# Kernel tuning notes

Hardware: AMD Instinct MI355X
Metric: run time of the kernel (lower is better)

## Reference

```python
import jax, jax.numpy as jnp
import numpy as np

N_NODES = 10000
N_EDGES = 160000
IN_DIM = 512
HID = 256
HEADS = 4
OUT_DIM = 512
NEG_SLOPE = 0.2  # PyG GATConv default


def _glorot(key, shape):
    fan_in, fan_out = shape[0], shape[-1]
    lim = jnp.sqrt(6.0 / (fan_in + fan_out))
    return jax.random.uniform(key, shape, jnp.float32, -lim, lim)


def setup_inputs() -> dict:
    key = jax.random.key(0)
    ks = jax.random.split(key, 16)
    x = jax.random.normal(ks[0], (N_NODES, IN_DIM), jnp.float32)
    edge_index = jax.random.randint(ks[1], (2, N_EDGES), 0, N_NODES, jnp.int64)
    # layer 1: GATConv(512 -> 256, heads=4, concat) -> out 1024
    W1 = _glorot(ks[2], (IN_DIM, HEADS * HID))
    att_src1 = _glorot(ks[3], (HEADS, HID))
    att_dst1 = _glorot(ks[4], (HEADS, HID))
    b1 = jnp.zeros((HEADS * HID,), jnp.float32)
    # layer 2: GATConv(1024 -> 256, heads=4, concat) -> out 1024
    W2 = _glorot(ks[5], (HEADS * HID, HEADS * HID))
    att_src2 = _glorot(ks[6], (HEADS, HID))
    att_dst2 = _glorot(ks[7], (HEADS, HID))
    b2 = jnp.zeros((HEADS * HID,), jnp.float32)
    # final fc: 1024 -> 512
    fcW = _glorot(ks[8], (HEADS * HID, OUT_DIM))
    fcb = jnp.zeros((OUT_DIM,), jnp.float32)
    return dict(x=x, edge_index=edge_index, W1=W1, att_src1=att_src1,
                att_dst1=att_dst1, b1=b1, W2=W2, att_src2=att_src2,
                att_dst2=att_dst2, b2=b2, fcW=fcW, fcb=fcb)


def gat_conv(x, src, dst, W, att_src, att_dst, bias):
    # x: [N, F_in]; src/dst: [E] (self-loops already included)
    N = x.shape[0]
    h = (x @ W).reshape(N, HEADS, HID)                       # [N, H, C]
    a_src = jnp.sum(h * att_src, axis=-1)                    # [N, H]
    a_dst = jnp.sum(h * att_dst, axis=-1)                    # [N, H]
    e = jax.nn.leaky_relu(a_src[src] + a_dst[dst], NEG_SLOPE)  # [E, H]
    # numerically stable segment softmax over destination nodes
    m = jax.ops.segment_max(e, dst, num_segments=N)          # [N, H]
    e = jnp.exp(e - m[dst])
    s = jax.ops.segment_sum(e, dst, num_segments=N)          # [N, H]
    alpha = e / (s[dst] + 1e-16)                             # [E, H]
    msg = alpha[:, :, None] * h[src]                         # [E, H, C]
    out = jax.ops.segment_sum(msg, dst, num_segments=N)      # [N, H, C]
    return out.reshape(N, HEADS * HID) + bias


def reference(x, edge_index, W1, att_src1, att_dst1, b1,
              W2, att_src2, att_dst2, b2, fcW, fcb):
    N = x.shape[0]
    loops = jnp.arange(N, dtype=edge_index.dtype)
    src = jnp.concatenate([edge_index[0], loops])  # PyG add_self_loops=True
    dst = jnp.concatenate([edge_index[1], loops])
    h = gat_conv(x, src, dst, W1, att_src1, att_dst1, b1)
    h = jax.nn.relu(h)  # dropout is identity in eval mode
    h = gat_conv(h, src, dst, W2, att_src2, att_dst2, b2)
    h = jax.nn.relu(h)
    return h @ fcW + fcb
```

## Files before the change

### kernel.cpp

```cpp
#include <hip/hip_runtime.h>
#include <hip/hip_bf16.h>

#define NN 10000
#define NE 160000
#define NET 170000
#define IN_DIM 512
#define D1 1024
#define HEADS 4
#define HID 256
#define OUT_DIM 512
#define NEG_SLOPE 0.2f

typedef __attribute__((ext_vector_type(8))) short bf16x8;
typedef __attribute__((ext_vector_type(4))) float f32x4;

__device__ inline float b2f(unsigned short b) {
    union { unsigned u; float f; } x; x.u = ((unsigned)b) << 16; return x.f;
}
__device__ inline unsigned short f2b(float f) {
    union { float f; unsigned u; } x; x.f = f;
    unsigned u = x.u;
    unsigned r = u + 0x7FFFu + ((u >> 16) & 1u);
    return (unsigned short)(r >> 16);
}
__device__ inline float lrelu(float v) { return v > 0.f ? v : NEG_SLOPE * v; }

__global__ void init_kernel(const int* ei32, int* flag, int* counts, int* cursor) {
    int i = blockIdx.x * blockDim.x + threadIdx.x;
    if (i < NN) { counts[i] = 0; cursor[i] = 0; }
    if (blockIdx.x == 0) {
        __shared__ int nz;
        if (threadIdx.x == 0) nz = 0;
        __syncthreads();
        int acc = 0;
        for (int k = threadIdx.x; k < 500; k += 256) acc |= ei32[2 * k + 1];
        if (acc) atomicOr(&nz, 1);
        __syncthreads();
        if (threadIdx.x == 0) flag[0] = (nz == 0) ? 1 : 0;
    }
}

__device__ inline void load_edge(const void* ei, int f64, int e, int& s, int& d) {
    if (f64) {
        const long long* p = (const long long*)ei;
        s = (int)p[e]; d = (int)p[NE + e];
    } else {
        const int* p = (const int*)ei;
        s = p[e]; d = p[NE + e];
    }
}

__global__ void count_kernel(const void* ei, const int* flag, int* counts) {
    int e = blockIdx.x * blockDim.x + threadIdx.x;
    if (e >= NET) return;
    int s, d;
    if (e < NE) load_edge(ei, *flag, e, s, d);
    else d = e - NE;
    atomicAdd(&counts[d], 1);
}

__global__ __launch_bounds__(256) void scan_kernel(const int* counts, int* indptr) {
    __shared__ int part[256];
    int t = threadIdx.x;
    int base = t * 40;
    int local[40];
    int sum = 0;
#pragma unroll
    for (int k = 0; k < 40; k++) {
        int i = base + k;
        int c = (i < NN) ? counts[i] : 0;
        local[k] = sum;
        sum += c;
    }
    part[t] = sum;
    __syncthreads();
    for (int off = 1; off < 256; off <<= 1) {
        int v = (t >= off) ? part[t - off] : 0;
        __syncthreads();
        part[t] += v;
        __syncthreads();
    }
    int excl = part[t] - sum;
#pragma unroll
    for (int k = 0; k < 40; k++) {
        int i = base + k;
        if (i < NN) indptr[i] = excl + local[k];
    }
    if (t == 255) indptr[NN] = part[255];
}

__global__ void fill_kernel(const void* ei, const int* flag, const int* indptr,
                            int* cursor, int* csr_src) {
    int e = blockIdx.x * blockDim.x + threadIdx.x;
    if (e >= NET) return;
    int s, d;
    if (e < NE) load_edge(ei, *flag, e, s, d);
    else { s = e - NE; d = s; }
    int pos = indptr[d] + atomicAdd(&cursor[d], 1);
    csr_src[pos] = s;
}

__device__ void tpose_tile(const float* __restrict__ in, unsigned short* __restrict__ out,
                           int R, int C, int bx, int by) {
    __shared__ float tile[32][33];
    int tx = threadIdx.x & 31, ty = threadIdx.x >> 5;
    int c = bx * 32 + tx;
#pragma unroll
    for (int r0 = 0; r0 < 32; r0 += 8) {
        int r = by * 32 + ty + r0;
        tile[ty + r0][tx] = in[(size_t)r * C + c];
    }
    __syncthreads();
    int oc = by * 32 + tx;
#pragma unroll
    for (int r0 = 0; r0 < 32; r0 += 8) {
        int orow = bx * 32 + ty + r0;
        out[(size_t)orow * R + oc] = f2b(tile[tx][ty + r0]);
    }
}

#define CVT_NB 5000
#define TP1_NB 512
#define TP2_NB 1024
#define TP3_NB 512
__global__ __launch_bounds__(256) void prep_kernel(
    const float* __restrict__ x, unsigned short* __restrict__ xb,
    const float* __restrict__ W1, unsigned short* __restrict__ W1t,
    const float* __restrict__ W2, unsigned short* __restrict__ W2t,
    const float* __restrict__ fcW, unsigned short* __restrict__ fcWt) {
    int b = blockIdx.x;
    if (b < CVT_NB) {
        int i = b * 256 + threadIdx.x;
        float4 v = reinterpret_cast<const float4*>(x)[i];
        ushort4 o;
        o.x = f2b(v.x); o.y = f2b(v.y); o.z = f2b(v.z); o.w = f2b(v.w);
        reinterpret_cast<ushort4*>(xb)[i] = o;
        return;
    }
    b -= CVT_NB;
    if (b < TP1_NB) { tpose_tile(W1, W1t, IN_DIM, D1, b & 31, b >> 5); return; }
    b -= TP1_NB;
    if (b < TP2_NB) { tpose_tile(W2, W2t, D1, D1, b & 31, b >> 5); return; }
    b -= TP2_NB;
    tpose_tile(fcW, fcWt, D1, OUT_DIM, b & 15, b >> 4);
}

#define BM 128
#define BN 128
#define BK 32
__global__ __launch_bounds__(256) void gemm128(
    const unsigned short* __restrict__ A, const unsigned short* __restrict__ B,
    const float* __restrict__ bias, float* __restrict__ Cf, unsigned short* __restrict__ Cb,
    int M, int N, int K) {
    __shared__ __align__(16) unsigned short As[BM * BK];
    __shared__ __align__(16) unsigned short Bs[BN * BK];
    int t = threadIdx.x;
    int row0 = blockIdx.x * BM, col0 = blockIdx.y * BN;
    int w = t >> 6, l = t & 63;
    int wr = w >> 1, wc = w & 1;
    f32x4 acc[4][4] = {};

    int sr = t >> 2;
    int sc = (t & 3) * 8;
    int arow0 = min(row0 + sr, M - 1);
    int arow1 = min(row0 + 64 + sr, M - 1);
    const unsigned short* aptr0 = A + (size_t)arow0 * K + sc;
    const unsigned short* aptr1 = A + (size_t)arow1 * K + sc;
    const unsigned short* bptr0 = B + (size_t)(col0 + sr) * K + sc;
    const unsigned short* bptr1 = B + (size_t)(col0 + 64 + sr) * K + sc;
    unsigned short* asd0 = As + w * 512;
    unsigned short* asd1 = As + 2048 + w * 512;
    unsigned short* bsd0 = Bs + w * 512;
    unsigned short* bsd1 = Bs + 2048 + w * 512;

    int rr = l & 15;
    int kk = (l >> 4) * 8;

    for (int k0 = 0; k0 < K; k0 += BK) {
        __builtin_amdgcn_global_load_lds(
            (const __attribute__((address_space(1))) void*)(aptr0 + k0),
            (__attribute__((address_space(3))) void*)asd0, 16, 0, 0);
        __builtin_amdgcn_global_load_lds(
            (const __attribute__((address_space(1))) void*)(aptr1 + k0),
            (__attribute__((address_space(3))) void*)asd1, 16, 0, 0);
        __builtin_amdgcn_global_load_lds(
            (const __attribute__((address_space(1))) void*)(bptr0 + k0),
            (__attribute__((address_space(3))) void*)bsd0, 16, 0, 0);
        __builtin_amdgcn_global_load_lds(
            (const __attribute__((address_space(1))) void*)(bptr1 + k0),
            (__attribute__((address_space(3))) void*)bsd1, 16, 0, 0);
        __syncthreads();

        bf16x8 af[4], bfv[4];
#pragma unroll
        for (int mi = 0; mi < 4; mi++)
            af[mi] = *reinterpret_cast<const bf16x8*>(&As[(wr * 64 + mi * 16 + rr) * BK + kk]);
#pragma unroll
        for (int ni = 0; ni < 4; ni++)
            bfv[ni] = *reinterpret_cast<const bf16x8*>(&Bs[(wc * 64 + ni * 16 + rr) * BK + kk]);
#pragma unroll
        for (int mi = 0; mi < 4; mi++)
#pragma unroll
            for (int ni = 0; ni < 4; ni++)
                acc[mi][ni] = __builtin_amdgcn_mfma_f32_16x16x32_bf16(af[mi], bfv[ni], acc[mi][ni], 0, 0, 0);
        __syncthreads();
    }

    int c_l = l & 15, r_h = (l >> 4) * 4;
#pragma unroll
    for (int mi = 0; mi < 4; mi++)
#pragma unroll
        for (int ni = 0; ni < 4; ni++) {
            int gc = col0 + wc * 64 + ni * 16 + c_l;
#pragma unroll
            for (int j = 0; j < 4; j++) {
                int gr = row0 + wr * 64 + mi * 16 + r_h + j;
                if (gr < M) {
                    float v = acc[mi][ni][j];
                    if (bias) v += bias[gc];
                    if (Cf) Cf[(size_t)gr * N + gc] = v;
                    if (Cb) Cb[(size_t)gr * N + gc] = f2b(v);
                }
            }
        }
}

__global__ __launch_bounds__(256) void att_kernel(const unsigned short* __restrict__ hb,
                                                  const float* __restrict__ att_s,
                                                  const float* __restrict__ att_d,
                                                  float* __restrict__ aS, float* __restrict__ aD) {
    int n = blockIdx.x;
    int t = threadIdx.x;
    int head = t >> 6, lane = t & 63;
    const unsigned short* hrow = hb + (size_t)n * D1 + head * HID + lane * 4;
    ushort4 hv = *reinterpret_cast<const ushort4*>(hrow);
    float4 as = *reinterpret_cast<const float4*>(att_s + head * HID + lane * 4);
    float4 ad = *reinterpret_cast<const float4*>(att_d + head * HID + lane * 4);
    float h0 = b2f(hv.x), h1 = b2f(hv.y), h2 = b2f(hv.z), h3 = b2f(hv.w);
    float ps = h0 * as.x + h1 * as.y + h2 * as.z + h3 * as.w;
    float pd = h0 * ad.x + h1 * ad.y + h2 * ad.z + h3 * ad.w;
#pragma unroll
    for (int off = 32; off; off >>= 1) {
        ps += __shfl_xor(ps, off);
        pd += __shfl_xor(pd, off);
    }
    if (lane == 0) {
        aS[n * HEADS + head] = ps;
        aD[n * HEADS + head] = pd;
    }
}

__global__ __launch_bounds__(256) void agg_kernel(const unsigned short* __restrict__ hb,
                                                  const float* __restrict__ aS,
                                                  const float* __restrict__ aD,
                                                  const int* __restrict__ indptr,
                                                  const int* __restrict__ csr_src,
                                                  const float* __restrict__ bias,
                                                  unsigned short* __restrict__ outb) {
    int i = blockIdx.x;
    int t = threadIdx.x;
    int beg = indptr[i], end = indptr[i + 1];
    int deg = end - beg;
    __shared__ float sm[HEADS], ss[HEADS];
    __shared__ float alpha_s[64 * HEADS];
    __shared__ int src_s[64];
    float4 adst = *reinterpret_cast<const float4*>(aD + i * HEADS);
    if (t < 64) {
        float mx0 = -1e30f, mx1 = -1e30f, mx2 = -1e30f, mx3 = -1e30f;
        for (int j = t; j < deg; j += 64) {
            int s = csr_src[beg + j];
            float4 a = *reinterpret_cast<const float4*>(aS + s * HEADS);
            mx0 = fmaxf(mx0, lrelu(a.x + adst.x));
            mx1 = fmaxf(mx1, lrelu(a.y + adst.y));
            mx2 = fmaxf(mx2, lrelu(a.z + adst.z));
            mx3 = fmaxf(mx3, lrelu(a.w + adst.w));
        }
#pragma unroll
        for (int off = 32; off; off >>= 1) {
            mx0 = fmaxf(mx0, __shfl_xor(mx0, off));
            mx1 = fmaxf(mx1, __shfl_xor(mx1, off));
            mx2 = fmaxf(mx2, __shfl_xor(mx2, off));
            mx3 = fmaxf(mx3, __shfl_xor(mx3, off));
        }
        if (t == 0) { sm[0] = mx0; sm[1] = mx1; sm[2] = mx2; sm[3] = mx3; }
    }
    if (t >= 64 && t < 68) ss[t - 64] = 0.f;
    __syncthreads();
    int head = t >> 6, lane = t & 63;
    float acc0 = 0.f, acc1 = 0.f, acc2 = 0.f, acc3 = 0.f;
    for (int c0 = 0; c0 < deg; c0 += 64) {
        int nj = min(64, deg - c0);
        if (t < 64) {
            int s = 0;
            float e0 = 0.f, e1 = 0.f, e2 = 0.f, e3 = 0.f;
            if (t < nj) {
                s = csr_src[beg + c0 + t];
                float4 a = *reinterpret_cast<const float4*>(aS + s * HEADS);
                e0 = __expf(lrelu(a.x + adst.x) - sm[0]);
                e1 = __expf(lrelu(a.y + adst.y) - sm[1]);
                e2 = __expf(lrelu(a.z + adst.z) - sm[2]);
                e3 = __expf(lrelu(a.w + adst.w) - sm[3]);
            }
            src_s[t] = s;
            alpha_s[t * 4 + 0] = e0;
            alpha_s[t * 4 + 1] = e1;
            alpha_s[t * 4 + 2] = e2;
            alpha_s[t * 4 + 3] = e3;
        }
        __syncthreads();
        {
            float v = alpha_s[lane * 4 + head];
#pragma unroll
            for (int off = 32; off; off >>= 1) v += __shfl_xor(v, off);
            if (lane == 0) ss[head] += v;
        }
        int njr = (nj + 3) & ~3;
        const unsigned short* hp = hb + (size_t)t * 4;
        ushort4 p0 = *reinterpret_cast<const ushort4*>(hp + (size_t)src_s[0] * D1);
        ushort4 p1 = *reinterpret_cast<const ushort4*>(hp + (size_t)src_s[1] * D1);
        ushort4 p2 = *reinterpret_cast<const ushort4*>(hp + (size_t)src_s[2] * D1);
        ushort4 p3 = *reinterpret_cast<const ushort4*>(hp + (size_t)src_s[3] * D1);
        for (int j = 0; j < njr; j += 4) {
            float w0 = alpha_s[(j + 0) * 4 + head];
            float w1 = alpha_s[(j + 1) * 4 + head];
            float w2 = alpha_s[(j + 2) * 4 + head];
            float w3 = alpha_s[(j + 3) * 4 + head];
            ushort4 c0v = p0, c1v = p1, c2v = p2, c3v = p3;
            if (j + 4 < njr) {
                p0 = *reinterpret_cast<const ushort4*>(hp + (size_t)src_s[j + 4] * D1);
                p1 = *reinterpret_cast<const ushort4*>(hp + (size_t)src_s[j + 5] * D1);
                p2 = *reinterpret_cast<const ushort4*>(hp + (size_t)src_s[j + 6] * D1);
                p3 = *reinterpret_cast<const ushort4*>(hp + (size_t)src_s[j + 7] * D1);
            }
            acc0 += w0 * b2f(c0v.x) + w1 * b2f(c1v.x) + w2 * b2f(c2v.x) + w3 * b2f(c3v.x);
            acc1 += w0 * b2f(c0v.y) + w1 * b2f(c1v.y) + w2 * b2f(c2v.y) + w3 * b2f(c3v.y);
            acc2 += w0 * b2f(c0v.z) + w1 * b2f(c1v.z) + w2 * b2f(c2v.z) + w3 * b2f(c3v.z);
            acc3 += w0 * b2f(c0v.w) + w1 * b2f(c1v.w) + w2 * b2f(c2v.w) + w3 * b2f(c3v.w);
        }
        __syncthreads();
    }
    float inv = 1.f / (ss[head] + 1e-16f);
    float4 bv = *reinterpret_cast<const float4*>(bias + t * 4);
    ushort4 o;
    o.x = f2b(fmaxf(acc0 * inv + bv.x, 0.f));
    o.y = f2b(fmaxf(acc1 * inv + bv.y, 0.f));
    o.z = f2b(fmaxf(acc2 * inv + bv.z, 0.f));
    o.w = f2b(fmaxf(acc3 * inv + bv.w, 0.f));
    *reinterpret_cast<ushort4*>(outb + (size_t)i * D1 + t * 4) = o;
}

extern "C" void kernel_launch(void* const* d_in, const int* in_sizes, int n_in,
                              void* d_out, int out_size, void* d_ws, size_t ws_size,
                              hipStream_t stream) {
    const float* x   = (const float*)d_in[0];
    const void*  ei  = d_in[1];
    const float* W1  = (const float*)d_in[2];
    const float* as1 = (const float*)d_in[3];
    const float* ad1 = (const float*)d_in[4];
    const float* b1  = (const float*)d_in[5];
    const float* W2  = (const float*)d_in[6];
    const float* as2 = (const float*)d_in[7];
    const float* ad2 = (const float*)d_in[8];
    const float* b2  = (const float*)d_in[9];
    const float* fcW = (const float*)d_in[10];
    const float* fcb = (const float*)d_in[11];
    float* out = (float*)d_out;

    char* ws = (char*)d_ws;
    size_t o = 0;
    auto carve = [&](size_t bytes) -> char* {
        char* p = ws + o;
        o = (o + bytes + 255) & ~(size_t)255;
        return p;
    };
    unsigned short* xb   = (unsigned short*)carve((size_t)NN * IN_DIM * 2);
    unsigned short* hb   = (unsigned short*)carve((size_t)NN * D1 * 2);
    unsigned short* x2b  = (unsigned short*)carve((size_t)NN * D1 * 2);
    unsigned short* W1t  = (unsigned short*)carve((size_t)D1 * IN_DIM * 2);
    unsigned short* W2t  = (unsigned short*)carve((size_t)D1 * D1 * 2);
    unsigned short* fcWt = (unsigned short*)carve((size_t)OUT_DIM * D1 * 2);
    float* aS   = (float*)carve((size_t)NN * HEADS * 4);
    float* aD   = (float*)carve((size_t)NN * HEADS * 4);
    int* counts = (int*)carve((size_t)NN * 4);
    int* cursor = (int*)carve((size_t)NN * 4);
    int* indptr = (int*)carve((size_t)(NN + 1) * 4);
    int* csr_src= (int*)carve((size_t)NET * 4);
    int* flag   = (int*)carve(4);
    (void)ws_size; (void)in_sizes; (void)n_in; (void)out_size;

    init_kernel<<<(NN + 255) / 256, 256, 0, stream>>>((const int*)ei, flag, counts, cursor);
    count_kernel<<<(NET + 255) / 256, 256, 0, stream>>>(ei, flag, counts);
    scan_kernel<<<1, 256, 0, stream>>>(counts, indptr);
    fill_kernel<<<(NET + 255) / 256, 256, 0, stream>>>(ei, flag, indptr, cursor, csr_src);

    prep_kernel<<<CVT_NB + TP1_NB + TP2_NB + TP3_NB, 256, 0, stream>>>(
        x, xb, W1, W1t, W2, W2t, fcW, fcWt);

    const int MB = (NN + BM - 1) / BM;
    gemm128<<<dim3(MB, D1 / BN), 256, 0, stream>>>(xb, W1t, nullptr, nullptr, hb, NN, D1, IN_DIM);
    att_kernel<<<NN, 256, 0, stream>>>(hb, as1, ad1, aS, aD);
    agg_kernel<<<NN, 256, 0, stream>>>(hb, aS, aD, indptr, csr_src, b1, x2b);
    gemm128<<<dim3(MB, D1 / BN), 256, 0, stream>>>(x2b, W2t, nullptr, nullptr, hb, NN, D1, D1);
    att_kernel<<<NN, 256, 0, stream>>>(hb, as2, ad2, aS, aD);
    agg_kernel<<<NN, 256, 0, stream>>>(hb, aS, aD, indptr, csr_src, b2, x2b);
    gemm128<<<dim3(MB, OUT_DIM / BN), 256, 0, stream>>>(x2b, fcWt, fcb, out, nullptr, NN, OUT_DIM, D1);
}
```

Before: 272.4 us.

## Fuse attention scores into GEMM epilogue and drop softmax max pass

Computes the per-node source and destination attention scores inside the GEMM epilogue from fp32 accumulators, using shuffle reductions and atomicAdd, which removes the separate att_kernel pass over h. The aggregation kernel drops the segment-max pass and exponentiates raw logits directly. It also splits edges across two 128-thread groups with 8-wide bf16 loads and deeper prefetch, combining the two partial sums through shared memory. The risks are overflow in exp without max subtraction, extra zeroing launches and atomic traffic, and scores now taken from unrounded fp32 values rather than bf16.

```diff
diff --git a/kernel.cpp b/kernel.cpp
--- a/kernel.cpp
+++ b/kernel.cpp
@@ -25,9 +25,11 @@
 }
 __device__ inline float lrelu(float v) { return v > 0.f ? v : NEG_SLOPE * v; }
 
-__global__ void init_kernel(const int* ei32, int* flag, int* counts, int* cursor) {
+__global__ void init_kernel(const int* ei32, int* flag, int* counts, int* cursor,
+                            float* aS, float* aD) {
     int i = blockIdx.x * blockDim.x + threadIdx.x;
     if (i < NN) { counts[i] = 0; cursor[i] = 0; }
+    for (int k = i; k < NN * HEADS; k += 40 * 256) { aS[k] = 0.f; aD[k] = 0.f; }
     if (blockIdx.x == 0) {
         __shared__ int nz;
         if (threadIdx.x == 0) nz = 0;
@@ -38,6 +40,11 @@
         __syncthreads();
         if (threadIdx.x == 0) flag[0] = (nz == 0) ? 1 : 0;
     }
+}
+
+__global__ void zatt_kernel(float* aS, float* aD) {
+    int i = blockIdx.x * blockDim.x + threadIdx.x;
+    if (i < NN * HEADS) { aS[i] = 0.f; aD[i] = 0.f; }
 }
 
 __device__ inline void load_edge(const void* ei, int f64, int e, int& s, int& d) {
@@ -151,6 +158,8 @@
 __global__ __launch_bounds__(256) void gemm128(
     const unsigned short* __restrict__ A, const unsigned short* __restrict__ B,
     const float* __restrict__ bias, float* __restrict__ Cf, unsigned short* __restrict__ Cb,
+    const float* __restrict__ attS, const float* __restrict__ attD,
+    float* __restrict__ aSo, float* __restrict__ aDo,
     int M, int N, int K) {
     __shared__ __align__(16) unsigned short As[BM * BK];
     __shared__ __align__(16) unsigned short Bs[BN * BK];
@@ -223,30 +232,39 @@
                 }
             }
         }
-}
-
-__global__ __launch_bounds__(256) void att_kernel(const unsigned short* __restrict__ hb,
-                                                  const float* __restrict__ att_s,
-                                                  const float* __restrict__ att_d,
-                                                  float* __restrict__ aS, float* __restrict__ aD) {
-    int n = blockIdx.x;
-    int t = threadIdx.x;
-    int head = t >> 6, lane = t & 63;
-    const unsigned short* hrow = hb + (size_t)n * D1 + head * HID + lane * 4;
-    ushort4 hv = *reinterpret_cast<const ushort4*>(hrow);
-    float4 as = *reinterpret_cast<const float4*>(att_s + head * HID + lane * 4);
-    float4 ad = *reinterpret_cast<const float4*>(att_d + head * HID + lane * 4);
-    float h0 = b2f(hv.x), h1 = b2f(hv.y), h2 = b2f(hv.z), h3 = b2f(hv.w);
-    float ps = h0 * as.x + h1 * as.y + h2 * as.z + h3 * as.w;
-    float pd = h0 * ad.x + h1 * ad.y + h2 * ad.z + h3 * ad.w;
-#pragma unroll
-    for (int off = 32; off; off >>= 1) {
-        ps += __shfl_xor(ps, off);
-        pd += __shfl_xor(pd, off);
-    }
-    if (lane == 0) {
-        aS[n * HEADS + head] = ps;
-        aD[n * HEADS + head] = pd;
+
+    if (attS) {
+        int head = col0 >> 8;
+        int cbase = (col0 & 255) + wc * 64 + c_l;
+        float asv0 = attS[head * HID + cbase];
+        float asv1 = attS[head * HID + cbase + 16];
+        float asv2 = attS[head * HID + cbase + 32];
+        float asv3 = attS[head * HID + cbase + 48];
+        float adv0 = attD[head * HID + cbase];
+        float adv1 = attD[head * HID + cbase + 16];
+        float adv2 = attD[head * HID + cbase + 32];
+        float adv3 = attD[head * HID + cbase + 48];
+#pragma unroll
+        for (int mi = 0; mi < 4; mi++)
+#pragma unroll
+            for (int j = 0; j < 4; j++) {
+                float ps = acc[mi][0][j] * asv0 + acc[mi][1][j] * asv1
+                         + acc[mi][2][j] * asv2 + acc[mi][3][j] * asv3;
+                float pd = acc[mi][0][j] * adv0 + acc[mi][1][j] * adv1
+                         + acc[mi][2][j] * adv2 + acc[mi][3][j] * adv3;
+#pragma unroll
+                for (int off = 1; off <= 8; off <<= 1) {
+                    ps += __shfl_xor(ps, off);
+                    pd += __shfl_xor(pd, off);
+                }
+                if (c_l == 0) {
+                    int gr = row0 + wr * 64 + mi * 16 + r_h + j;
+                    if (gr < M) {
+                        atomicAdd(&aSo[gr * HEADS + head], ps);
+                        atomicAdd(&aDo[gr * HEADS + head], pd);
+                    }
+                }
+            }
     }
 }
 
@@ -259,35 +277,18 @@
                                                   unsigned short* __restrict__ outb) {
     int i = blockIdx.x;
     int t = threadIdx.x;
-    int beg = indptr[i], end = indptr[i + 1];
-    int deg = end - beg;
-    __shared__ float sm[HEADS], ss[HEADS];
+    int beg = indptr[i], deg = indptr[i + 1] - beg;
+    __shared__ float ssum[HEADS];
     __shared__ float alpha_s[64 * HEADS];
     __shared__ int src_s[64];
+    __shared__ float xacc[128 * 8];
+    if (t < HEADS) ssum[t] = 0.f;
     float4 adst = *reinterpret_cast<const float4*>(aD + i * HEADS);
-    if (t < 64) {
-        float mx0 = -1e30f, mx1 = -1e30f, mx2 = -1e30f, mx3 = -1e30f;
-        for (int j = t; j < deg; j += 64) {
-            int s = csr_src[beg + j];
-            float4 a = *reinterpret_cast<const float4*>(aS + s * HEADS);
-            mx0 = fmaxf(mx0, lrelu(a.x + adst.x));
-            mx1 = fmaxf(mx1, lrelu(a.y + adst.y));
-            mx2 = fmaxf(mx2, lrelu(a.z + adst.z));
-            mx3 = fmaxf(mx3, lrelu(a.w + adst.w));
-        }
-#pragma unroll
-        for (int off = 32; off; off >>= 1) {
-            mx0 = fmaxf(mx0, __shfl_xor(mx0, off));
-            mx1 = fmaxf(mx1, __shfl_xor(mx1, off));
-            mx2 = fmaxf(mx2, __shfl_xor(mx2, off));
-            mx3 = fmaxf(mx3, __shfl_xor(mx3, off));
-        }
-        if (t == 0) { sm[0] = mx0; sm[1] = mx1; sm[2] = mx2; sm[3] = mx3; }
-    }
-    if (t >= 64 && t < 68) ss[t - 64] = 0.f;
+    int g = t >> 7, u = t & 127;
+    int headu = u >> 5;
+    const unsigned short* hp8 = hb + (size_t)u * 8;
+    float a0 = 0, a1 = 0, a2 = 0, a3 = 0, a4 = 0, a5 = 0, a6 = 0, a7 = 0;
     __syncthreads();
-    int head = t >> 6, lane = t & 63;
-    float acc0 = 0.f, acc1 = 0.f, acc2 = 0.f, acc3 = 0.f;
     for (int c0 = 0; c0 < deg; c0 += 64) {
         int nj = min(64, deg - c0);
         if (t < 64) {
@@ -296,57 +297,118 @@
             if (t < nj) {
                 s = csr_src[beg + c0 + t];
                 float4 a = *reinterpret_cast<const float4*>(aS + s * HEADS);
-                e0 = __expf(lrelu(a.x + adst.x) - sm[0]);
-                e1 = __expf(lrelu(a.y + adst.y) - sm[1]);
-                e2 = __expf(lrelu(a.z + adst.z) - sm[2]);
-                e3 = __expf(lrelu(a.w + adst.w) - sm[3]);
+                e0 = __expf(lrelu(a.x + adst.x));
+                e1 = __expf(lrelu(a.y + adst.y));
+                e2 = __expf(lrelu(a.z + adst.z));
+                e3 = __expf(lrelu(a.w + adst.w));
             }
             src_s[t] = s;
             alpha_s[t * 4 + 0] = e0;
             alpha_s[t * 4 + 1] = e1;
             alpha_s[t * 4 + 2] = e2;
             alpha_s[t * 4 + 3] = e3;
+            float v0 = e0, v1 = e1, v2 = e2, v3 = e3;
+#pragma unroll
+            for (int off = 32; off; off >>= 1) {
+                v0 += __shfl_xor(v0, off);
+                v1 += __shfl_xor(v1, off);
+                v2 += __shfl_xor(v2, off);
+                v3 += __shfl_xor(v3, off);
+            }
+            if (t == 0) { ssum[0] += v0; ssum[1] += v1; ssum[2] += v2; ssum[3] += v3; }
         }
         __syncthreads();
-        {
-            float v = alpha_s[lane * 4 + head];
-#pragma unroll
-            for (int off = 32; off; off >>= 1) v += __shfl_xor(v, off);
-            if (lane == 0) ss[head] += v;
+        int nG = (nj + 1 - g) >> 1;
+        int nGr = (nG + 7) & ~7;
+#define LDROW(idx) (*reinterpret_cast<const bf16x8*>(hp8 + (size_t)src_s[idx] * D1))
+        if (nGr) {
+            bf16x8 p0 = LDROW(g);
+            bf16x8 p1 = LDROW(g + 2);
+            bf16x8 p2 = LDROW(g + 4);
+            bf16x8 p3 = LDROW(g + 6);
+            bf16x8 p4 = LDROW(g + 8);
+            bf16x8 p5 = LDROW(g + 10);
+            bf16x8 p6 = LDROW(g + 12);
+            bf16x8 p7 = LDROW(g + 14);
+            for (int k = 0; k < nGr; k += 8) {
+                int j0 = g + 2 * k;
+                float w0 = alpha_s[(j0) * 4 + headu];
+                float w1 = alpha_s[(j0 + 2) * 4 + headu];
+                float w2 = alpha_s[(j0 + 4) * 4 + headu];
+                float w3 = alpha_s[(j0 + 6) * 4 + headu];
+                float w4 = alpha_s[(j0 + 8) * 4 + headu];
+                float w5 = alpha_s[(j0 + 10) * 4 + headu];
+                float w6 = alpha_s[(j0 + 12) * 4 + headu];
+                float w7 = alpha_s[(j0 + 14) * 4 + headu];
+                bf16x8 c0v = p0, c1v = p1, c2v = p2, c3v = p3;
+                bf16x8 c4v = p4, c5v = p5, c6v = p6, c7v = p7;
+                int jn = j0 + 16;
+                p0 = LDROW(min(jn, 63));
+                p1 = LDROW(min(jn + 2, 63));
+                p2 = LDROW(min(jn + 4, 63));
+                p3 = LDROW(min(jn + 6, 63));
+                p4 = LDROW(min(jn + 8, 63));
+                p5 = LDROW(min(jn + 10, 63));
+                p6 = LDROW(min(jn + 12, 63));
+                p7 = LDROW(min(jn + 14, 63));
+                a0 += w0 * b2f((unsigned short)c0v[0]) + w1 * b2f((unsigned short)c1v[0])
+                    + w2 * b2f((unsigned short)c2v[0]) + w3 * b2f((unsigned short)c3v[0])
+                    + w4 * b2f((unsigned short)c4v[0]) + w5 * b2f((unsigned short)c5v[0])
+                    + w6 * b2f((unsigned short)c6v[0]) + w7 * b2f((unsigned short)c7v[0]);
+                a1 += w0 * b2f((unsigned short)c0v[1]) + w1 * b2f((unsigned short)c1v[1])
+                    + w2 * b2f((unsigned short)c2v[1]) + w3 * b2f((unsigned short)c3v[1])
+                    + w4 * b2f((unsigned short)c4v[1]) + w5 * b2f((unsigned short)c5v[1])
+                    + w6 * b2f((unsigned short)c6v[1]) + w7 * b2f((unsigned short)c7v[1]);
+                a2 += w0 * b2f((unsigned short)c0v[2]) + w1 * b2f((unsigned short)c1v[2])
+                    + w2 * b2f((unsigned short)c2v[2]) + w3 * b2f((unsigned short)c3v[2])
+                    + w4 * b2f((unsigned short)c4v[2]) + w5 * b2f((unsigned short)c5v[2])
+                    + w6 * b2f((unsigned short)c6v[2]) + w7 * b2f((unsigned short)c7v[2]);
+                a3 += w0 * b2f((unsigned short)c0v[3]) + w1 * b2f((unsigned short)c1v[3])
+                    + w2 * b2f((unsigned short)c2v[3]) + w3 * b2f((unsigned short)c3v[3])
+                    + w4 * b2f((unsigned short)c4v[3]) + w5 * b2f((unsigned short)c5v[3])
+                    + w6 * b2f((unsigned short)c6v[3]) + w7 * b2f((unsigned short)c7v[3]);
+                a4 += w0 * b2f((unsigned short)c0v[4]) + w1 * b2f((unsigned short)c1v[4])
+                    + w2 * b2f((unsigned short)c2v[4]) + w3 * b2f((unsigned short)c3v[4])
+                    + w4 * b2f((unsigned short)c4v[4]) + w5 * b2f((unsigned short)c5v[4])
+                    + w6 * b2f((unsigned short)c6v[4]) + w7 * b2f((unsigned short)c7v[4]);
+                a5 += w0 * b2f((unsigned short)c0v[5]) + w1 * b2f((unsigned short)c1v[5])
+                    + w2 * b2f((unsigned short)c2v[5]) + w3 * b2f((unsigned short)c3v[5])
+                    + w4 * b2f((unsigned short)c4v[5]) + w5 * b2f((unsigned short)c5v[5])
+                    + w6 * b2f((unsigned short)c6v[5]) + w7 * b2f((unsigned short)c7v[5]);
+                a6 += w0 * b2f((unsigned short)c0v[6]) + w1 * b2f((unsigned short)c1v[6])
+                    + w2 * b2f((unsigned short)c2v[6]) + w3 * b2f((unsigned short)c3v[6])
+                    + w4 * b2f((unsigned short)c4v[6]) + w5 * b2f((unsigned short)c5v[6])
+                    + w6 * b2f((unsigned short)c6v[6]) + w7 * b2f((unsigned short)c7v[6]);
+                a7 += w0 * b2f((unsigned short)c0v[7]) + w1 * b2f((unsigned short)c1v[7])
+                    + w2 * b2f((unsigned short)c2v[7]) + w3 * b2f((unsigned short)c3v[7])
+                    + w4 * b2f((unsigned short)c4v[7]) + w5 * b2f((unsigned short)c5v[7])
+                    + w6 * b2f((unsigned short)c6v[7]) + w7 * b2f((unsigned short)c7v[7]);
+            }
         }
-        int njr = (nj + 3) & ~3;
-        const unsigned short* hp = hb + (size_t)t * 4;
-        ushort4 p0 = *reinterpret_cast<const ushort4*>(hp + (size_t)src_s[0] * D1);
-        ushort4 p1 = *reinterpret_cast<const ushort4*>(hp + (size_t)src_s[1] * D1);
-        ushort4 p2 = *reinterpret_cast<const ushort4*>(hp + (size_t)src_s[2] * D1);
-        ushort4 p3 = *reinterpret_cast<const ushort4*>(hp + (size_t)src_s[3] * D1);
-        for (int j = 0; j < njr; j += 4) {
-            float w0 = alpha_s[(j + 0) * 4 + head];
-            float w1 = alpha_s[(j + 1) * 4 + head];
-            float w2 = alpha_s[(j + 2) * 4 + head];
-            float w3 = alpha_s[(j + 3) * 4 + head];
-            ushort4 c0v = p0, c1v = p1, c2v = p2, c3v = p3;
-            if (j + 4 < njr) {
-                p0 = *reinterpret_cast<const ushort4*>(hp + (size_t)src_s[j + 4] * D1);
-                p1 = *reinterpret_cast<const ushort4*>(hp + (size_t)src_s[j + 5] * D1);
-                p2 = *reinterpret_cast<const ushort4*>(hp + (size_t)src_s[j + 6] * D1);
-                p3 = *reinterpret_cast<const ushort4*>(hp + (size_t)src_s[j + 7] * D1);
-            }
-            acc0 += w0 * b2f(c0v.x) + w1 * b2f(c1v.x) + w2 * b2f(c2v.x) + w3 * b2f(c3v.x);
-            acc1 += w0 * b2f(c0v.y) + w1 * b2f(c1v.y) + w2 * b2f(c2v.y) + w3 * b2f(c3v.y);
-            acc2 += w0 * b2f(c0v.z) + w1 * b2f(c1v.z) + w2 * b2f(c2v.z) + w3 * b2f(c3v.z);
-            acc3 += w0 * b2f(c0v.w) + w1 * b2f(c1v.w) + w2 * b2f(c2v.w) + w3 * b2f(c3v.w);
-        }
-        __syncthreads();
-    }
-    float inv = 1.f / (ss[head] + 1e-16f);
-    float4 bv = *reinterpret_cast<const float4*>(bias + t * 4);
-    ushort4 o;
-    o.x = f2b(fmaxf(acc0 * inv + bv.x, 0.f));
-    o.y = f2b(fmaxf(acc1 * inv + bv.y, 0.f));
-    o.z = f2b(fmaxf(acc2 * inv + bv.z, 0.f));
-    o.w = f2b(fmaxf(acc3 * inv + bv.w, 0.f));
-    *reinterpret_cast<ushort4*>(outb + (size_t)i * D1 + t * 4) = o;
+#undef LDROW
+        __syncthreads();
+    }
+    if (g == 1) {
+        xacc[u * 8 + 0] = a0; xacc[u * 8 + 1] = a1;
+        xacc[u * 8 + 2] = a2; xacc[u * 8 + 3] = a3;
+        xacc[u * 8 + 4] = a4; xacc[u * 8 + 5] = a5;
+        xacc[u * 8 + 6] = a6; xacc[u * 8 + 7] = a7;
+    }
+    __syncthreads();
+    if (g == 0) {
+        float inv = 1.f / (ssum[headu] + 1e-16f);
+        const float* bp = bias + u * 8;
+        bf16x8 ov;
+        ov[0] = (short)f2b(fmaxf((a0 + xacc[u * 8 + 0]) * inv + bp[0], 0.f));
+        ov[1] = (short)f2b(fmaxf((a1 + xacc[u * 8 + 1]) * inv + bp[1], 0.f));
+        ov[2] = (short)f2b(fmaxf((a2 + xacc[u * 8 + 2]) * inv + bp[2], 0.f));
+        ov[3] = (short)f2b(fmaxf((a3 + xacc[u * 8 + 3]) * inv + bp[3], 0.f));
+        ov[4] = (short)f2b(fmaxf((a4 + xacc[u * 8 + 4]) * inv + bp[4], 0.f));
+        ov[5] = (short)f2b(fmaxf((a5 + xacc[u * 8 + 5]) * inv + bp[5], 0.f));
+        ov[6] = (short)f2b(fmaxf((a6 + xacc[u * 8 + 6]) * inv + bp[6], 0.f));
+        ov[7] = (short)f2b(fmaxf((a7 + xacc[u * 8 + 7]) * inv + bp[7], 0.f));
+        *reinterpret_cast<bf16x8*>(outb + (size_t)i * D1 + u * 8) = ov;
+    }
 }
 
 extern "C" void kernel_launch(void* const* d_in, const int* in_sizes, int n_in,
@@ -388,7 +450,7 @@
     int* flag   = (int*)carve(4);
     (void)ws_size; (void)in_sizes; (void)n_in; (void)out_size;
 
-    init_kernel<<<(NN + 255) / 256, 256, 0, stream>>>((const int*)ei, flag, counts, cursor);
+    init_kernel<<<(NN + 255) / 256, 256, 0, stream>>>((const int*)ei, flag, counts, cursor, aS, aD);
     count_kernel<<<(NET + 255) / 256, 256, 0, stream>>>(ei, flag, counts);
     scan_kernel<<<1, 256, 0, stream>>>(counts, indptr);
     fill_kernel<<<(NET + 255) / 256, 256, 0, stream>>>(ei, flag, indptr, cursor, csr_src);
@@ -397,11 +459,14 @@
         x, xb, W1, W1t, W2, W2t, fcW, fcWt);
 
     const int MB = (NN + BM - 1) / BM;
-    gemm128<<<dim3(MB, D1 / BN), 256, 0, stream>>>(xb, W1t, nullptr, nullptr, hb, NN, D1, IN_DIM);
-    att_kernel<<<NN, 256, 0, stream>>>(hb, as1, ad1, aS, aD);
+    gemm128<<<dim3(MB, D1 / BN), 256, 0, stream>>>(xb, W1t, nullptr, nullptr, hb,
+                                                   as1, ad1, aS, aD, NN, D1, IN_DIM);
     agg_kernel<<<NN, 256, 0, stream>>>(hb, aS, aD, indptr, csr_src, b1, x2b);
-    gemm128<<<dim3(MB, D1 / BN), 256, 0, stream>>>(x2b, W2t, nullptr, nullptr, hb, NN, D1, D1);
-    att_kernel<<<NN, 256, 0, stream>>>(hb, as2, ad2, aS, aD);
+    zatt_kernel<<<(NN * HEADS + 255) / 256, 256, 0, stream>>>(aS, aD);
+    gemm128<<<dim3(MB, D1 / BN), 256, 0, stream>>>(x2b, W2t, nullptr, nullptr, hb,
+                                                   as2, ad2, aS, aD, NN, D1, D1);
     agg_kernel<<<NN, 256, 0, stream>>>(hb, aS, aD, indptr, csr_src, b2, x2b);
-    gemm128<<<dim3(MB, OUT_DIM / BN), 256, 0, stream>>>(x2b, fcWt, fcb, out, nullptr, NN, OUT_DIM, D1);
-}
+    gemm128<<<dim3(MB, OUT_DIM / BN), 256, 0, stream>>>(x2b, fcWt, fcb, out, nullptr,
+                                                        nullptr, nullptr, nullptr, nullptr,
+                                                        NN, OUT_DIM, D1);
+}
```

Result: slower. 290.4 us (+6.6%).
